# Kernel tuning notes

Measured on AMD Instinct MI355X. Metric: run time of the kernel, lower is better.

The kernel has to match this reference:

```python
import jax, jax.numpy as jnp
import numpy as np
import math

B, S, D, H, F = 2, 2048, 1024, 16, 4096
HD = D // H
EPS = 1e-5

def _alibi_slopes(n_heads):
    # n_heads is a power of 2 here (16): m_i = start * start**i, start = 2^(-2^(-(log2(n)-3)))
    start = 2.0 ** (-(2.0 ** (-(math.log2(n_heads) - 3))))
    return np.array([start * (start ** i) for i in range(n_heads)], dtype=np.float32)

SLOPES = jnp.asarray(_alibi_slopes(H))  # (H,)


def setup_inputs() -> dict:
    key = jax.random.key(0)
    ks = jax.random.split(key, 8)
    s = 0.02
    return {
        "x":  jax.random.normal(ks[0], (B, S, D), jnp.float32),
        "Wq": jax.random.normal(ks[1], (D, D), jnp.float32) * s,
        "Wk": jax.random.normal(ks[2], (D, D), jnp.float32) * s,
        "Wv": jax.random.normal(ks[3], (D, D), jnp.float32) * s,
        "Wo": jax.random.normal(ks[4], (D, D), jnp.float32) * s,
        "bo": jnp.zeros((D,), jnp.float32),
        "W1": jax.random.normal(ks[5], (F, D), jnp.float32) * s,
        "b1": jnp.zeros((F,), jnp.float32),
        "W2": jax.random.normal(ks[6], (D, F), jnp.float32) * s,
        "b2": jnp.zeros((D,), jnp.float32),
        "g1": jnp.ones((D,), jnp.float32),
        "be1": jnp.zeros((D,), jnp.float32),
        "g2": jnp.ones((D,), jnp.float32),
        "be2": jnp.zeros((D,), jnp.float32),
    }


def _layernorm(h, g, b):
    mu = jnp.mean(h, axis=-1, keepdims=True)
    var = jnp.mean((h - mu) ** 2, axis=-1, keepdims=True)
    return (h - mu) * jax.lax.rsqrt(var + EPS) * g + b


def reference(x, Wq, Wk, Wv, Wo, bo, W1, b1, W2, b2, g1, be1, g2, be2):
    # --- pre-norm ALiBi attention ---
    h = _layernorm(x, g1, be1)
    q = (h @ Wq.T).reshape(B, S, H, HD).transpose(0, 2, 1, 3)  # (B,H,S,HD)
    k = (h @ Wk.T).reshape(B, S, H, HD).transpose(0, 2, 1, 3)
    v = (h @ Wv.T).reshape(B, S, H, HD).transpose(0, 2, 1, 3)
    scores = jnp.einsum("bhqd,bhkd->bhqk", q, k) / math.sqrt(HD)
    pos = jnp.arange(S)
    dist = (pos[None, :] - pos[:, None]).astype(jnp.float32)      # (S,S): j - i
    bias = SLOPES[:, None, None] * dist[None, :, :]               # (H,S,S)
    attn = jax.nn.softmax(scores + bias[None], axis=-1)
    ao = jnp.einsum("bhqk,bhkd->bhqd", attn, v)
    ao = ao.transpose(0, 2, 1, 3).reshape(B, S, D) @ Wo.T + bo
    x = x + ao
    # --- pre-norm FFN ---
    h2 = _layernorm(x, g2, be2)
    ff = jax.nn.relu(h2 @ W1.T + b1) @ W2.T + b2
    return x + ff
```

## Files before the change

### kernel.cpp

```cpp
#include <hip/hip_runtime.h>
#include <hip/hip_bf16.h>
#include <stdint.h>

typedef unsigned short u16;
typedef __attribute__((ext_vector_type(8))) short short8;
typedef __attribute__((ext_vector_type(4))) float f32x4;

#define S_LEN 2048
#define D_DIM 1024
#define NHEAD 16
#define HDIM 64
#define NROWS 4096

__device__ __forceinline__ u16 f2bf(float f) {
  union { float f; uint32_t u; } c; c.f = f;
  uint32_t r = (c.u + 0x7fffu + ((c.u >> 16) & 1u)) >> 16;
  return (u16)r;
}

__device__ __forceinline__ uint32_t pack_bf2(float a, float b) {
  __hip_bfloat162 h = __float22bfloat162_rn(float2{a, b});
  union { __hip_bfloat162 h; uint32_t u; } c; c.h = h;
  return c.u;
}

__device__ __forceinline__ void gload_lds16(const void* g, void* l) {
  typedef const __attribute__((address_space(1))) unsigned int gq_t;
  typedef __attribute__((address_space(3))) unsigned int lq_t;
  __builtin_amdgcn_global_load_lds((gq_t*)(uintptr_t)g,
                                   (lq_t*)(uint32_t)(uintptr_t)l, 16, 0, 0);
}

__global__ __launch_bounds__(256) void cast_all(const float* __restrict__ Wq,
                                                const float* __restrict__ Wk,
                                                const float* __restrict__ Wv,
                                                const float* __restrict__ Wo,
                                                const float* __restrict__ W1,
                                                const float* __restrict__ W2,
                                                u16* __restrict__ wqkv,
                                                u16* __restrict__ wo,
                                                u16* __restrict__ w1,
                                                u16* __restrict__ w2) {
  int i = blockIdx.x * 256 + threadIdx.x;
  const float* src;
  u16* dst;
  int rel;
  if (i < 786432) {
    int ws = i / 262144;
    rel = i - ws * 262144;
    src = (ws == 0) ? Wq : ((ws == 1) ? Wk : Wv);
    dst = wqkv + (size_t)ws * 1048576;
  } else if (i < 1048576) {
    rel = i - 786432; src = Wo; dst = wo;
  } else if (i < 2097152) {
    rel = i - 1048576; src = W1; dst = w1;
  } else {
    rel = i - 2097152; src = W2; dst = w2;
  }
  float4 v = ((const float4*)src)[rel];
  ((ushort4*)dst)[rel] = make_ushort4(f2bf(v.x), f2bf(v.y), f2bf(v.z), f2bf(v.w));
}

__global__ __launch_bounds__(256) void ln_kernel(const float* __restrict__ x,
                                                 const float* __restrict__ g,
                                                 const float* __restrict__ be,
                                                 u16* __restrict__ out) {
  int row = blockIdx.x;
  int tid = threadIdx.x;
  const float4 v = ((const float4*)(x + (size_t)row * D_DIM))[tid];
  float s = v.x + v.y + v.z + v.w;
  float s2 = v.x * v.x + v.y * v.y + v.z * v.z + v.w * v.w;
#pragma unroll
  for (int off = 1; off < 64; off <<= 1) {
    s += __shfl_xor(s, off);
    s2 += __shfl_xor(s2, off);
  }
  __shared__ float ss[4], ss2[4];
  if ((tid & 63) == 0) { ss[tid >> 6] = s; ss2[tid >> 6] = s2; }
  __syncthreads();
  s = ss[0] + ss[1] + ss[2] + ss[3];
  s2 = ss2[0] + ss2[1] + ss2[2] + ss2[3];
  float mu = s * (1.0f / D_DIM);
  float var = s2 * (1.0f / D_DIM) - mu * mu;
  float rs = rsqrtf(var + 1e-5f);
  float4 gv = ((const float4*)g)[tid];
  float4 bv = ((const float4*)be)[tid];
  ushort4 o = make_ushort4(f2bf((v.x - mu) * rs * gv.x + bv.x),
                           f2bf((v.y - mu) * rs * gv.y + bv.y),
                           f2bf((v.z - mu) * rs * gv.z + bv.z),
                           f2bf((v.w - mu) * rs * gv.w + bv.w));
  ((ushort4*)(out + (size_t)row * D_DIM))[tid] = o;
}

template <int EPI>
__global__ __launch_bounds__(512, 2) void gemm_bt2(const u16* __restrict__ A,
                                                   const u16* __restrict__ Bw,
                                                   void* __restrict__ Cout,
                                                   const float* __restrict__ bias,
                                                   int M, int N, int K) {
  __shared__ u16 lsA[2][256 * 32];
  __shared__ u16 lsB[2][256 * 32];
  const int tid = threadIdx.x;
  const int wid = tid >> 6, lane = tid & 63;
  const int l4 = lane & 15, lh = lane >> 4;
  const int wr = wid >> 2, wc = wid & 3;
  const int nbn = N >> 8;
  const int nwg = (M >> 8) * nbn;
  const int t0 = (blockIdx.x & 7) * (nwg >> 3) + (blockIdx.x >> 3);
  const int bm = t0 / nbn, bn = t0 % nbn;

  f32x4 acc[8][4];
#pragma unroll
  for (int i = 0; i < 8; ++i)
#pragma unroll
    for (int j = 0; j < 4; ++j) acc[i][j] = (f32x4){0.f, 0.f, 0.f, 0.f};

  const int srow = lane >> 2;
  const int sblk = (lane & 3) ^ ((lane >> 3) & 3);
  const u16* Abase = A + ((size_t)bm * 256 + wid * 32 + srow) * K + sblk * 8;
  const u16* Bbase = Bw + ((size_t)bn * 256 + wid * 32 + srow) * K + sblk * 8;
  const size_t r16 = (size_t)16 * K;
#define STAGE(BUF, KT)                                              \
  {                                                                 \
    int ko = (KT) * 32;                                             \
    gload_lds16(Abase + ko, (char*)lsA[BUF] + wid * 2048);          \
    gload_lds16(Abase + r16 + ko, (char*)lsA[BUF] + wid * 2048 + 1024); \
    gload_lds16(Bbase + ko, (char*)lsB[BUF] + wid * 2048);          \
    gload_lds16(Bbase + r16 + ko, (char*)lsB[BUF] + wid * 2048 + 1024); \
  }

  const int swz = (lh ^ ((l4 >> 1) & 3)) << 4;
  int aoff[8], boff[4];
#pragma unroll
  for (int m = 0; m < 8; ++m) aoff[m] = (wr * 128 + m * 16 + l4) * 64 + swz;
#pragma unroll
  for (int n = 0; n < 4; ++n) boff[n] = (wc * 64 + n * 16 + l4) * 64 + swz;

  STAGE(0, 0);
  __syncthreads();
  int cur = 0;
  const int NT = K >> 5;

  for (int t = 0; t < NT; ++t) {
    if (t + 1 < NT) STAGE(cur ^ 1, t + 1);
    const char* La = (const char*)lsA[cur];
    const char* Lb = (const char*)lsB[cur];
    short8 aF[4], bF[4], aG[4];
#pragma unroll
    for (int m = 0; m < 4; ++m) aF[m] = *(const short8*)(La + aoff[m]);
#pragma unroll
    for (int n = 0; n < 4; ++n) bF[n] = *(const short8*)(Lb + boff[n]);
    __builtin_amdgcn_s_setprio(1);
#pragma unroll
    for (int m = 0; m < 4; ++m)
#pragma unroll
      for (int n = 0; n < 4; ++n)
        acc[m][n] = __builtin_amdgcn_mfma_f32_16x16x32_bf16(aF[m], bF[n], acc[m][n], 0, 0, 0);
    __builtin_amdgcn_s_setprio(0);
#pragma unroll
    for (int m = 0; m < 4; ++m) aG[m] = *(const short8*)(La + aoff[m + 4]);
    __builtin_amdgcn_s_setprio(1);
#pragma unroll
    for (int m = 0; m < 4; ++m)
#pragma unroll
      for (int n = 0; n < 4; ++n)
        acc[m + 4][n] = __builtin_amdgcn_mfma_f32_16x16x32_bf16(aG[m], bF[n], acc[m + 4][n], 0, 0, 0);
    __builtin_amdgcn_s_setprio(0);
    if (t + 1 < NT) __syncthreads();
    cur ^= 1;
  }

  const int row0 = bm * 256 + wr * 128 + lh * 4;
  const int col0 = bn * 256 + wc * 64 + l4;
#pragma unroll
  for (int m = 0; m < 8; ++m) {
#pragma unroll
    for (int n = 0; n < 4; ++n) {
      int col = col0 + n * 16;
#pragma unroll
      for (int r = 0; r < 4; ++r) {
        size_t idx = (size_t)(row0 + m * 16 + r) * N + col;
        float v = acc[m][n][r];
        if (EPI == 0) {
          ((u16*)Cout)[idx] = f2bf(v);
        } else {
          v += bias[col];
          ((u16*)Cout)[idx] = f2bf(v > 0.f ? v : 0.f);
        }
      }
    }
  }
#undef STAGE
}

template <int EPI>
__global__ __launch_bounds__(256) void gemm_bt(const u16* __restrict__ A,
                                               const u16* __restrict__ Bw,
                                               void* __restrict__ Cout,
                                               const float* __restrict__ bias,
                                               const float* __restrict__ resid,
                                               int M, int N, int K, int ksl) {
  __shared__ u16 lsA[128 * 64];
  __shared__ u16 lsB[128 * 64];
  const int tid = threadIdx.x;
  const int wid = tid >> 6, lane = tid & 63;
  const int l4 = lane & 15, lh = lane >> 4;
  const int nbn = N >> 7;
  const int nwgs = (M >> 7) * nbn;
  const int slice = blockIdx.x / nwgs;
  const int id0 = blockIdx.x % nwgs;
  const int t = (id0 & 7) * (nwgs >> 3) + (id0 >> 3);
  const int bm = t / nbn, bn = t % nbn;
  const int wr = wid >> 1, wc = wid & 1;
  const int Ks = K / ksl;

  f32x4 acc[4][4];
#pragma unroll
  for (int i = 0; i < 4; ++i)
#pragma unroll
    for (int j = 0; j < 4; ++j) acc[i][j] = (f32x4){0.f, 0.f, 0.f, 0.f};

  const u16* Ab = A + (size_t)bm * 128 * K + (size_t)slice * Ks;
  const u16* Bb = Bw + (size_t)bn * 128 * K + (size_t)slice * Ks;
  const int srow = (lane >> 3);
  const int scol = (lane & 7) * 8;

  for (int k0 = 0; k0 < Ks; k0 += 64) {
#pragma unroll
    for (int c = 0; c < 4; ++c) {
      int ch = wid * 4 + c;
      int row = ch * 8 + srow;
      gload_lds16(Ab + (size_t)row * K + k0 + scol, &lsA[ch * 512]);
      gload_lds16(Bb + (size_t)row * K + k0 + scol, &lsB[ch * 512]);
    }
    __syncthreads();
#pragma unroll
    for (int ks = 0; ks < 2; ++ks) {
      short8 af[4], bf[4];
#pragma unroll
      for (int i = 0; i < 4; ++i) {
        af[i] = *(const short8*)&lsA[(wr * 64 + i * 16 + l4) * 64 + ks * 32 + lh * 8];
        bf[i] = *(const short8*)&lsB[(wc * 64 + i * 16 + l4) * 64 + ks * 32 + lh * 8];
      }
#pragma unroll
      for (int i = 0; i < 4; ++i)
#pragma unroll
        for (int j = 0; j < 4; ++j)
          acc[i][j] = __builtin_amdgcn_mfma_f32_16x16x32_bf16(af[i], bf[j], acc[i][j], 0, 0, 0);
    }
    __syncthreads();
  }

  const int row0 = bm * 128 + wr * 64;
  const int col0 = bn * 128 + wc * 64;
  float* Cp = (float*)Cout + (size_t)slice * M * N;
#pragma unroll
  for (int i = 0; i < 4; ++i) {
#pragma unroll
    for (int j = 0; j < 4; ++j) {
      int col = col0 + j * 16 + l4;
#pragma unroll
      for (int r = 0; r < 4; ++r) {
        int row = row0 + i * 16 + lh * 4 + r;
        size_t idx = (size_t)row * N + col;
        float v = acc[i][j][r];
        if (EPI == 1) {
          ((float*)Cout)[idx] = v + bias[col] + resid[idx];
        } else {
          Cp[idx] = v;
        }
      }
    }
  }
}

__global__ __launch_bounds__(256) void reduce2_kernel(const float* __restrict__ p0,
                                                      const float* __restrict__ p1,
                                                      const float* __restrict__ resid,
                                                      const float* __restrict__ bias,
                                                      float* __restrict__ out) {
  for (int i = blockIdx.x * 256 + threadIdx.x; i < (NROWS * D_DIM) / 4;
       i += gridDim.x * 256) {
    float4 a = ((const float4*)p0)[i];
    float4 b = ((const float4*)p1)[i];
    float4 r = ((const float4*)resid)[i];
    float4 bb = ((const float4*)bias)[i & 255];
    float4 o;
    o.x = a.x + b.x + r.x + bb.x;
    o.y = a.y + b.y + r.y + bb.y;
    o.z = a.z + b.z + r.z + bb.z;
    o.w = a.w + b.w + r.w + bb.w;
    ((float4*)out)[i] = o;
  }
}

__global__ __launch_bounds__(256) void transpose_v(const u16* __restrict__ qkv,
                                                   u16* __restrict__ vt) {
  const int gw = blockIdx.x * 4 + (threadIdx.x >> 6);
  const int lane = threadIdx.x & 63;
  const int bh = gw >> 5;
  const int st = gw & 31;
  const int b = bh >> 4, h = bh & 15;
  const u16* src = qkv + (size_t)(b * S_LEN + st * 64) * 3072 + 2048 + h * 64 + lane;
  short8 acc8[8];
#pragma unroll
  for (int o = 0; o < 8; ++o)
#pragma unroll
    for (int i = 0; i < 8; ++i)
      acc8[o][i] = (short)src[(size_t)(o * 8 + i) * 3072];
  u16* dst = vt + ((size_t)bh * 64 + lane) * S_LEN + st * 64;
#pragma unroll
  for (int o = 0; o < 8; ++o) *(short8*)(dst + o * 8) = acc8[o];
}

__global__ __launch_bounds__(256, 4) void attn_kernel(const u16* __restrict__ qkv,
                                                      const u16* __restrict__ vt,
                                                      u16* __restrict__ ao,
                                                      float* __restrict__ pO,
                                                      float* __restrict__ pML) {
  const int id = blockIdx.x;
  const int sub = id & 63;
  const int ugrp = id >> 6;
  int h, j;
  if (ugrp < 15) { h = 15 - ugrp / 3; j = ugrp % 3; }
  else if (ugrp < 19) { h = 10 - ((ugrp - 15) >> 1); j = (ugrp - 15) & 1; }
  else { h = 27 - ugrp; j = 0; }
  const int b = sub >> 5, qt = sub & 31;
  const int bh = b * 16 + h;
  const int tid = threadIdx.x;
  const int wid = tid >> 6, lane = tid & 63;
  const int l4 = lane & 15, lh = lane >> 4;

  __shared__ u16 Kt[2][64 * 64];
  __shared__ u16 Vt[2][64 * 64];
  __shared__ u16 Pt[4][16 * 64];

  const size_t RS = 3 * D_DIM;
  const u16* base = qkv + (size_t)b * S_LEN * RS + h * HDIM;
  const u16* kbase = base + D_DIM;
  const u16* vtb = vt + (size_t)bh * HDIM * S_LEN;
  char* PtW = (char*)Pt[wid];

  short8 qf[2];
  {
    const u16* qp = base + (size_t)(qt * 64 + wid * 16 + l4) * RS + lh * 8;
    qf[0] = *(const short8*)qp;
    qf[1] = *(const short8*)(qp + 32);
  }

  int koff[4][2];
#pragma unroll
  for (int nb = 0; nb < 4; ++nb)
#pragma unroll
    for (int ks = 0; ks < 2; ++ks) {
      int row = nb * 16 + l4;
      koff[nb][ks] = row * 128 + (((ks * 32 + lh * 8) * 2) ^ ((row & 7) << 4));
    }
  int poff[2];
#pragma unroll
  for (int ks = 0; ks < 2; ++ks)
    poff[ks] = l4 * 128 + (((ks * 64 + lh * 16)) ^ ((l4 & 7) << 4));
  int pwoff[4];
#pragma unroll
  for (int nb = 0; nb < 4; ++nb)
    pwoff[nb] = l4 * 128 + (((lh * 8 + nb * 32)) ^ ((l4 & 7) << 4));

  const float slope2 = exp2f(-0.5f * (float)(h + 1)) * 1.44269504088896f;
  const float scale2 = 0.125f * 1.44269504088896f;
  const int ibase = lh * 4 - (qt * 64 + wid * 16 + l4);
  float bc[4][4];
#pragma unroll
  for (int nb = 0; nb < 4; ++nb)
#pragma unroll
    for (int r = 0; r < 4; ++r)
      bc[nb][r] = slope2 * (float)(ibase + 16 * nb + r);

  int nt = (int)ceilf(40.0f / (64.0f * slope2)) + 1;
  if (nt > 32) nt = 32;
  const int nsp = (nt + 11) / 12;
  const int ktmin = 32 - nt;
  const int hi = 31 - j * 12;
  int lo = hi - 11;
  if (lo < ktmin) lo = ktmin;

  float m = -1e30f;
  f32x4 lacc = (f32x4){0.f, 0.f, 0.f, 0.f};
  f32x4 accO[4];
#pragma unroll
  for (int nd = 0; nd < 4; ++nd) accO[nd] = (f32x4){0.f, 0.f, 0.f, 0.f};
  const short8 vones = {(short)0x3F80, (short)0x3F80, (short)0x3F80, (short)0x3F80,
                        (short)0x3F80, (short)0x3F80, (short)0x3F80, (short)0x3F80};

  const int srow = tid >> 3;
  const int sc8 = (tid & 7) * 8;
  const int swo = srow * 128 + ((sc8 * 2) ^ ((srow & 7) << 4));
  short8 kreg[2], vreg[2];
#define STAGE_LOAD(KT)                                                              \
  {                                                                                 \
    kreg[0] = *(const short8*)(kbase + (size_t)((KT)*64 + srow) * RS + sc8);        \
    kreg[1] = *(const short8*)(kbase + (size_t)((KT)*64 + srow + 32) * RS + sc8);   \
    vreg[0] = *(const short8*)(vtb + (size_t)srow * S_LEN + (KT)*64 + sc8);         \
    vreg[1] = *(const short8*)(vtb + (size_t)(srow + 32) * S_LEN + (KT)*64 + sc8);  \
  }
#define STAGE_WRITE(B)                                   \
  {                                                      \
    *(short8*)((char*)Kt[B] + swo) = kreg[0];            \
    *(short8*)((char*)Kt[B] + swo + 4096) = kreg[1];     \
    *(short8*)((char*)Vt[B] + swo) = vreg[0];            \
    *(short8*)((char*)Vt[B] + swo + 4096) = vreg[1];     \
  }

  STAGE_LOAD(hi);
  STAGE_WRITE(0);
  __syncthreads();
  int cur = 0;
  float ktoff = slope2 * 64.0f * (float)hi;
  const float dko = slope2 * 64.0f;

  for (int kt = hi; kt >= lo; --kt) {
    if (kt > lo) STAGE_LOAD(kt - 1);
    const char* Kc = (const char*)Kt[cur];
    const char* Vc = (const char*)Vt[cur];

    f32x4 sacc[4];
#pragma unroll
    for (int nb = 0; nb < 4; ++nb) sacc[nb] = (f32x4){0.f, 0.f, 0.f, 0.f};
    __builtin_amdgcn_s_setprio(1);
#pragma unroll
    for (int ks = 0; ks < 2; ++ks)
#pragma unroll
      for (int nb = 0; nb < 4; ++nb) {
        short8 kf = *(const short8*)(Kc + koff[nb][ks]);
        sacc[nb] = __builtin_amdgcn_mfma_f32_16x16x32_bf16(kf, qf[ks], sacc[nb], 0, 0, 0);
      }
    __builtin_amdgcn_s_setprio(0);

    float p[4][4];
#pragma unroll
    for (int nb = 0; nb < 4; ++nb)
#pragma unroll
      for (int r = 0; r < 4; ++r)
        p[nb][r] = fmaf(sacc[nb][r], scale2, bc[nb][r]);

    float mx0 = fmaxf(fmaxf(p[0][0], p[0][1]), fmaxf(p[0][2], p[0][3]));
    float mx1 = fmaxf(fmaxf(p[1][0], p[1][1]), fmaxf(p[1][2], p[1][3]));
    float mx2 = fmaxf(fmaxf(p[2][0], p[2][1]), fmaxf(p[2][2], p[2][3]));
    float mx3 = fmaxf(fmaxf(p[3][0], p[3][1]), fmaxf(p[3][2], p[3][3]));
    float tm = fmaxf(fmaxf(mx0, mx1), fmaxf(mx2, mx3));
    tm = fmaxf(tm, __shfl_xor(tm, 16));
    tm = fmaxf(tm, __shfl_xor(tm, 32));

    float mm = m - ktoff;
    if (__any(tm > mm)) {
      float mn = fmaxf(mm, tm);
      float corr = exp2f(mm - mn);
      m = mn + ktoff;
      mm = mn;
      float cb[4];
#pragma unroll
      for (int r = 0; r < 4; ++r)
        cb[r] = __shfl(corr, (lane & 48) | (lh * 4 + r));
#pragma unroll
      for (int nd = 0; nd < 4; ++nd)
#pragma unroll
        for (int r = 0; r < 4; ++r) accO[nd][r] *= cb[r];
#pragma unroll
      for (int r = 0; r < 4; ++r) lacc[r] *= cb[r];
    }

#pragma unroll
    for (int nb = 0; nb < 4; ++nb)
#pragma unroll
      for (int r = 0; r < 4; ++r) p[nb][r] = exp2f(p[nb][r] - mm);

#pragma unroll
    for (int nb = 0; nb < 4; ++nb) {
      uint32_t w0 = pack_bf2(p[nb][0], p[nb][1]);
      uint32_t w1 = pack_bf2(p[nb][2], p[nb][3]);
      *(uint2*)(PtW + pwoff[nb]) = make_uint2(w0, w1);
    }
    asm volatile("s_waitcnt lgkmcnt(0)" ::: "memory");

    __builtin_amdgcn_s_setprio(1);
#pragma unroll
    for (int ks = 0; ks < 2; ++ks) {
      short8 pf = *(const short8*)(PtW + poff[ks]);
      lacc = __builtin_amdgcn_mfma_f32_16x16x32_bf16(pf, vones, lacc, 0, 0, 0);
#pragma unroll
      for (int nd = 0; nd < 4; ++nd) {
        short8 vf = *(const short8*)(Vc + koff[nd][ks]);
        accO[nd] = __builtin_amdgcn_mfma_f32_16x16x32_bf16(pf, vf, accO[nd], 0, 0, 0);
      }
    }
    __builtin_amdgcn_s_setprio(0);

    if (kt > lo) STAGE_WRITE(cur ^ 1);
    __syncthreads();
    cur ^= 1;
    ktoff -= dko;
  }

  if (nsp == 1) {
    float ib[4];
#pragma unroll
    for (int r = 0; r < 4; ++r) ib[r] = 1.0f / lacc[r];
    u16* aop = ao + ((size_t)(b * S_LEN + qt * 64 + wid * 16 + lh * 4)) * D_DIM + h * HDIM;
#pragma unroll
    for (int nd = 0; nd < 4; ++nd)
#pragma unroll
      for (int r = 0; r < 4; ++r)
        aop[(size_t)r * D_DIM + nd * 16 + l4] = f2bf(accO[nd][r] * ib[r]);
  } else {
    const int sbase = (h <= 10) ? (h - 9) * 2 : 4 + (h - 11) * 3;
    const int pidx = sub * 19 + sbase + j;
    float* Op = pO + (size_t)pidx * 4096;
#pragma unroll
    for (int nd = 0; nd < 4; ++nd)
#pragma unroll
      for (int r = 0; r < 4; ++r)
        Op[(wid * 16 + lh * 4 + r) * 64 + nd * 16 + l4] = accO[nd][r];
    float mq[4];
#pragma unroll
    for (int r = 0; r < 4; ++r)
      mq[r] = __shfl(m, (lane & 48) | (lh * 4 + r));
    if (l4 == 0) {
      float* mlp = pML + (size_t)pidx * 128 + (wid * 16 + lh * 4) * 2;
#pragma unroll
      for (int r = 0; r < 4; ++r) {
        mlp[r * 2] = mq[r];
        mlp[r * 2 + 1] = lacc[r];
      }
    }
  }
#undef STAGE_LOAD
#undef STAGE_WRITE
}

__global__ __launch_bounds__(256) void attn_combine(const float* __restrict__ pO,
                                                    const float* __restrict__ pML,
                                                    u16* __restrict__ ao) {
  const int g = blockIdx.x;
  const int sub = g & 63;
  const int h = 9 + (g >> 6);
  const int b = sub >> 5, qt = sub & 31;
  const int nsp = (h <= 10) ? 2 : 3;
  const int sbase = (h <= 10) ? (h - 9) * 2 : 4 + (h - 11) * 3;
  const int pidx0 = sub * 19 + sbase;
  const int tid = threadIdx.x;
  const int row = tid >> 2;
  const int d0 = (tid & 3) * 16;

  float mj[3], lj[3];
#pragma unroll
  for (int k = 0; k < 3; ++k) { mj[k] = -1e30f; lj[k] = 0.f; }
  for (int k = 0; k < nsp; ++k) {
    mj[k] = pML[(size_t)(pidx0 + k) * 128 + row * 2];
    lj[k] = pML[(size_t)(pidx0 + k) * 128 + row * 2 + 1];
  }
  float ms = fmaxf(mj[0], fmaxf(mj[1], mj[2]));
  float w[3];
  float lsum = 0.f;
#pragma unroll
  for (int k = 0; k < 3; ++k) {
    w[k] = exp2f(mj[k] - ms);
    lsum += w[k] * lj[k];
  }
  float inv = 1.0f / lsum;

  u16* aop = ao + ((size_t)(b * S_LEN + qt * 64 + row)) * D_DIM + h * HDIM + d0;
#pragma unroll
  for (int c = 0; c < 4; ++c) {
    float4 o = {0.f, 0.f, 0.f, 0.f};
    for (int k = 0; k < nsp; ++k) {
      const float4 v = *(const float4*)(pO + (size_t)(pidx0 + k) * 4096 + row * 64 + d0 + c * 4);
      o.x += w[k] * v.x; o.y += w[k] * v.y; o.z += w[k] * v.z; o.w += w[k] * v.w;
    }
    ushort4 u4 = make_ushort4(f2bf(o.x * inv), f2bf(o.y * inv), f2bf(o.z * inv), f2bf(o.w * inv));
    *(ushort4*)(aop + c * 4) = u4;
  }
}

extern "C" void kernel_launch(void* const* d_in, const int* in_sizes, int n_in,
                              void* d_out, int out_size, void* d_ws, size_t ws_size,
                              hipStream_t stream) {
  const float* x   = (const float*)d_in[0];
  const float* Wq  = (const float*)d_in[1];
  const float* Wk  = (const float*)d_in[2];
  const float* Wv  = (const float*)d_in[3];
  const float* Wo  = (const float*)d_in[4];
  const float* bo  = (const float*)d_in[5];
  const float* W1  = (const float*)d_in[6];
  const float* b1  = (const float*)d_in[7];
  const float* W2  = (const float*)d_in[8];
  const float* b2  = (const float*)d_in[9];
  const float* g1  = (const float*)d_in[10];
  const float* be1 = (const float*)d_in[11];
  const float* g2  = (const float*)d_in[12];
  const float* be2 = (const float*)d_in[13];

  char* p = (char*)d_ws;
  u16* wqkv = (u16*)p; p += (size_t)3072 * 1024 * 2;
  u16* wo   = (u16*)p; p += (size_t)1024 * 1024 * 2;
  u16* w1   = (u16*)p; p += (size_t)4096 * 1024 * 2;
  u16* w2   = (u16*)p; p += (size_t)4096 * 1024 * 2;
  u16* hb   = (u16*)p; p += (size_t)4096 * 1024 * 2;
  u16* qkvb = (u16*)p; p += (size_t)4096 * 3072 * 2;
  u16* aob  = (u16*)p; p += (size_t)4096 * 1024 * 2;
  float* x1 = (float*)p; p += (size_t)4096 * 1024 * 4;
  u16* h2b  = (u16*)p; p += (size_t)4096 * 1024 * 2;
  u16* ff1  = (u16*)p; p += (size_t)4096 * 4096 * 2;
  u16* vt   = ff1;
  float* pO = (float*)(ff1 + (size_t)4 * 1024 * 1024);
  float* pML = pO + (size_t)1216 * 4096;
  float* pk = (float*)hb;

  cast_all<<<12288, 256, 0, stream>>>(Wq, Wk, Wv, Wo, W1, W2, wqkv, wo, w1, w2);

  ln_kernel<<<4096, 256, 0, stream>>>(x, g1, be1, hb);
  gemm_bt2<0><<<16 * 12, 512, 0, stream>>>(hb, wqkv, qkvb, nullptr, 4096, 3072, 1024);
  transpose_v<<<256, 256, 0, stream>>>(qkvb, vt);
  attn_kernel<<<1792, 256, 0, stream>>>(qkvb, vt, aob, pO, pML);
  attn_combine<<<448, 256, 0, stream>>>(pO, pML, aob);
  gemm_bt<1><<<32 * 8, 256, 0, stream>>>(aob, wo, x1, bo, x, 4096, 1024, 1024, 1);
  ln_kernel<<<4096, 256, 0, stream>>>(x1, g2, be2, h2b);
  gemm_bt2<2><<<16 * 16, 512, 0, stream>>>(h2b, w1, ff1, b1, 4096, 4096, 1024);
  gemm_bt<3><<<2 * 32 * 8, 256, 0, stream>>>(ff1, w2, pk, nullptr, nullptr, 4096, 1024, 4096, 2);
  reduce2_kernel<<<2048, 256, 0, stream>>>(pk, pk + (size_t)4096 * 1024, x1, b2, (float*)d_out);
}
```

Baseline: 236.3 us.

## Add 256x128-tile 512-thread double-buffered GEMM for FFN down-projection

Introduces a new GEMM kernel with 256x128 output tiles, 8 waves, K-step 32 and a double-buffered LDS pipeline using direct global-to-LDS loads. It replaces the 128x128 kernel for the W2 split-K GEMM. The larger M tile raises reuse of the B operand and halves the workgroup count. The cost is more registers per thread and fewer workgroups (256) to spread across CUs.

New measurement: 234.7 us. No clear change (-0.7%).

```diff
diff --git a/kernel.cpp b/kernel.cpp
--- a/kernel.cpp
+++ b/kernel.cpp
@@ -194,6 +194,101 @@
 }
 
 template <int EPI>
+__global__ __launch_bounds__(512, 2) void gemm_bt3(const u16* __restrict__ A,
+                                                   const u16* __restrict__ Bw,
+                                                   void* __restrict__ Cout,
+                                                   const float* __restrict__ bias,
+                                                   const float* __restrict__ resid,
+                                                   int M, int N, int K, int ksl) {
+  __shared__ u16 lsA[2][256 * 32];
+  __shared__ u16 lsB[2][128 * 32];
+  const int tid = threadIdx.x;
+  const int wid = tid >> 6, lane = tid & 63;
+  const int l4 = lane & 15, lh = lane >> 4;
+  const int wr = wid >> 1, wc = wid & 1;
+  const int nbn = N >> 7;
+  const int nwgs = (M >> 8) * nbn;
+  const int slice = blockIdx.x / nwgs;
+  const int id0 = blockIdx.x % nwgs;
+  const int t0 = (id0 & 7) * (nwgs >> 3) + (id0 >> 3);
+  const int bm = t0 / nbn, bn = t0 % nbn;
+  const int Ks = K / ksl;
+
+  f32x4 acc[4][4];
+#pragma unroll
+  for (int i = 0; i < 4; ++i)
+#pragma unroll
+    for (int j = 0; j < 4; ++j) acc[i][j] = (f32x4){0.f, 0.f, 0.f, 0.f};
+
+  const int srow = lane >> 2;
+  const int sblk = (lane & 3) ^ ((lane >> 3) & 3);
+  const u16* Abase = A + ((size_t)bm * 256 + wid * 16 + srow) * K + (size_t)slice * Ks + sblk * 8;
+  const u16* Bbase = Bw + ((size_t)bn * 128 + wid * 16 + srow) * K + (size_t)slice * Ks + sblk * 8;
+  const size_t r128 = (size_t)128 * K;
+#define STAGE(BUF, KT)                                               \
+  {                                                                  \
+    int ko = (KT) * 32;                                              \
+    gload_lds16(Abase + ko, (char*)lsA[BUF] + wid * 1024);           \
+    gload_lds16(Abase + r128 + ko, (char*)lsA[BUF] + 8192 + wid * 1024); \
+    gload_lds16(Bbase + ko, (char*)lsB[BUF] + wid * 1024);           \
+  }
+
+  const int swz = (lh ^ ((l4 >> 1) & 3)) << 4;
+  int aoff[4], boff[4];
+#pragma unroll
+  for (int m = 0; m < 4; ++m) aoff[m] = (wr * 64 + m * 16 + l4) * 64 + swz;
+#pragma unroll
+  for (int n = 0; n < 4; ++n) boff[n] = (wc * 64 + n * 16 + l4) * 64 + swz;
+
+  STAGE(0, 0);
+  __syncthreads();
+  int cur = 0;
+  const int NT = Ks >> 5;
+
+  for (int t = 0; t < NT; ++t) {
+    if (t + 1 < NT) STAGE(cur ^ 1, t + 1);
+    const char* La = (const char*)lsA[cur];
+    const char* Lb = (const char*)lsB[cur];
+    short8 aF[4], bF[4];
+#pragma unroll
+    for (int m = 0; m < 4; ++m) aF[m] = *(const short8*)(La + aoff[m]);
+#pragma unroll
+    for (int n = 0; n < 4; ++n) bF[n] = *(const short8*)(Lb + boff[n]);
+    __builtin_amdgcn_s_setprio(1);
+#pragma unroll
+    for (int m = 0; m < 4; ++m)
+#pragma unroll
+      for (int n = 0; n < 4; ++n)
+        acc[m][n] = __builtin_amdgcn_mfma_f32_16x16x32_bf16(aF[m], bF[n], acc[m][n], 0, 0, 0);
+    __builtin_amdgcn_s_setprio(0);
+    if (t + 1 < NT) __syncthreads();
+    cur ^= 1;
+  }
+
+  const int row0 = bm * 256 + wr * 64 + lh * 4;
+  const int col0 = bn * 128 + wc * 64 + l4;
+  float* Cp = (float*)Cout + (size_t)slice * M * N;
+#pragma unroll
+  for (int m = 0; m < 4; ++m) {
+#pragma unroll
+    for (int n = 0; n < 4; ++n) {
+      int col = col0 + n * 16;
+#pragma unroll
+      for (int r = 0; r < 4; ++r) {
+        size_t idx = (size_t)(row0 + m * 16 + r) * N + col;
+        float v = acc[m][n][r];
+        if (EPI == 1) {
+          ((float*)Cout)[idx] = v + bias[col] + resid[idx];
+        } else {
+          Cp[idx] = v;
+        }
+      }
+    }
+  }
+#undef STAGE
+}
+
+template <int EPI>
 __global__ __launch_bounds__(256) void gemm_bt(const u16* __restrict__ A,
                                                const u16* __restrict__ Bw,
                                                void* __restrict__ Cout,
@@ -624,6 +719,6 @@
   gemm_bt<1><<<32 * 8, 256, 0, stream>>>(aob, wo, x1, bo, x, 4096, 1024, 1024, 1);
   ln_kernel<<<4096, 256, 0, stream>>>(x1, g2, be2, h2b);
   gemm_bt2<2><<<16 * 16, 512, 0, stream>>>(h2b, w1, ff1, b1, 4096, 4096, 1024);
-  gemm_bt<3><<<2 * 32 * 8, 256, 0, stream>>>(ff1, w2, pk, nullptr, nullptr, 4096, 1024, 4096, 2);
+  gemm_bt3<3><<<2 * 16 * 8, 512, 0, stream>>>(ff1, w2, pk, nullptr, nullptr, 4096, 1024, 4096, 2);
   reduce2_kernel<<<2048, 256, 0, stream>>>(pk, pk + (size_t)4096 * 1024, x1, b2, (float*)d_out);
 }
```

## Run FFN down-projection on 256x256 GEMM with split-K 4 and bf16 partials

Applied to the files above, without the earlier changes.

The second FFN GEMM (K=4096) moves from the 128x128 split-K-2 kernel with fp32 partials to the larger 256x256 double-buffered kernel. That kernel gains a split-K parameter, and this call uses 4 slices. Partial sums are now stored in bf16, and a new vectorized reduce kernel adds the 4 slices plus bias and residual. The aim is better MFMA data reuse and full-GPU occupancy on the long-K GEMM without more partial-sum traffic. The cost is reduced accuracy from rounding each partial to bf16, plus one workgroup per CU.

Measured after the change: 227.5 us. -3.7%, faster.

```diff
diff --git a/kernel.cpp b/kernel.cpp
--- a/kernel.cpp
+++ b/kernel.cpp
@@ -16,6 +16,11 @@
   union { float f; uint32_t u; } c; c.f = f;
   uint32_t r = (c.u + 0x7fffu + ((c.u >> 16) & 1u)) >> 16;
   return (u16)r;
+}
+
+__device__ __forceinline__ float bf2f(u16 v) {
+  union { uint32_t u; float f; } c; c.u = ((uint32_t)v) << 16;
+  return c.f;
 }
 
 __device__ __forceinline__ uint32_t pack_bf2(float a, float b) {
@@ -97,7 +102,7 @@
                                                    const u16* __restrict__ Bw,
                                                    void* __restrict__ Cout,
                                                    const float* __restrict__ bias,
-                                                   int M, int N, int K) {
+                                                   int M, int N, int K, int ksl) {
   __shared__ u16 lsA[2][256 * 32];
   __shared__ u16 lsB[2][256 * 32];
   const int tid = threadIdx.x;
@@ -106,8 +111,11 @@
   const int wr = wid >> 2, wc = wid & 3;
   const int nbn = N >> 8;
   const int nwg = (M >> 8) * nbn;
-  const int t0 = (blockIdx.x & 7) * (nwg >> 3) + (blockIdx.x >> 3);
+  const int slice = blockIdx.x / nwg;
+  const int id0 = blockIdx.x % nwg;
+  const int t0 = (id0 & 7) * (nwg >> 3) + (id0 >> 3);
   const int bm = t0 / nbn, bn = t0 % nbn;
+  const int Ks = K / ksl;
 
   f32x4 acc[8][4];
 #pragma unroll
@@ -117,8 +125,8 @@
 
   const int srow = lane >> 2;
   const int sblk = (lane & 3) ^ ((lane >> 3) & 3);
-  const u16* Abase = A + ((size_t)bm * 256 + wid * 32 + srow) * K + sblk * 8;
-  const u16* Bbase = Bw + ((size_t)bn * 256 + wid * 32 + srow) * K + sblk * 8;
+  const u16* Abase = A + ((size_t)bm * 256 + wid * 32 + srow) * K + (size_t)slice * Ks + sblk * 8;
+  const u16* Bbase = Bw + ((size_t)bn * 256 + wid * 32 + srow) * K + (size_t)slice * Ks + sblk * 8;
   const size_t r16 = (size_t)16 * K;
 #define STAGE(BUF, KT)                                              \
   {                                                                 \
@@ -139,7 +147,7 @@
   STAGE(0, 0);
   __syncthreads();
   int cur = 0;
-  const int NT = K >> 5;
+  const int NT = Ks >> 5;
 
   for (int t = 0; t < NT; ++t) {
     if (t + 1 < NT) STAGE(cur ^ 1, t + 1);
@@ -172,6 +180,7 @@
 
   const int row0 = bm * 256 + wr * 128 + lh * 4;
   const int col0 = bn * 256 + wc * 64 + l4;
+  u16* Cp = (u16*)Cout + (size_t)slice * M * N;
 #pragma unroll
   for (int m = 0; m < 8; ++m) {
 #pragma unroll
@@ -183,9 +192,11 @@
         float v = acc[m][n][r];
         if (EPI == 0) {
           ((u16*)Cout)[idx] = f2bf(v);
-        } else {
+        } else if (EPI == 2) {
           v += bias[col];
           ((u16*)Cout)[idx] = f2bf(v > 0.f ? v : 0.f);
+        } else {
+          Cp[idx] = f2bf(v);
         }
       }
     }
@@ -274,24 +285,29 @@
   }
 }
 
-__global__ __launch_bounds__(256) void reduce2_kernel(const float* __restrict__ p0,
-                                                      const float* __restrict__ p1,
+__global__ __launch_bounds__(256) void reduce4_kernel(const u16* __restrict__ pk,
                                                       const float* __restrict__ resid,
                                                       const float* __restrict__ bias,
                                                       float* __restrict__ out) {
-  for (int i = blockIdx.x * 256 + threadIdx.x; i < (NROWS * D_DIM) / 4;
-       i += gridDim.x * 256) {
-    float4 a = ((const float4*)p0)[i];
-    float4 b = ((const float4*)p1)[i];
-    float4 r = ((const float4*)resid)[i];
-    float4 bb = ((const float4*)bias)[i & 255];
-    float4 o;
-    o.x = a.x + b.x + r.x + bb.x;
-    o.y = a.y + b.y + r.y + bb.y;
-    o.z = a.z + b.z + r.z + bb.z;
-    o.w = a.w + b.w + r.w + bb.w;
-    ((float4*)out)[i] = o;
-  }
+  const size_t SL = (size_t)NROWS * D_DIM;
+  int i = blockIdx.x * 256 + threadIdx.x;
+  short8 p0 = *(const short8*)(pk + (size_t)i * 8);
+  short8 p1 = *(const short8*)(pk + SL + (size_t)i * 8);
+  short8 p2 = *(const short8*)(pk + 2 * SL + (size_t)i * 8);
+  short8 p3 = *(const short8*)(pk + 3 * SL + (size_t)i * 8);
+  int col = (i * 8) & (D_DIM - 1);
+  float4 b0 = *(const float4*)(bias + col);
+  float4 b1 = *(const float4*)(bias + col + 4);
+  float4 r0 = ((const float4*)resid)[i * 2];
+  float4 r1 = ((const float4*)resid)[i * 2 + 1];
+  float o[8];
+#pragma unroll
+  for (int j = 0; j < 8; ++j)
+    o[j] = bf2f((u16)p0[j]) + bf2f((u16)p1[j]) + bf2f((u16)p2[j]) + bf2f((u16)p3[j]);
+  float4 w0 = {o[0] + b0.x + r0.x, o[1] + b0.y + r0.y, o[2] + b0.z + r0.z, o[3] + b0.w + r0.w};
+  float4 w1 = {o[4] + b1.x + r1.x, o[5] + b1.y + r1.y, o[6] + b1.z + r1.z, o[7] + b1.w + r1.w};
+  ((float4*)out)[i * 2] = w0;
+  ((float4*)out)[i * 2 + 1] = w1;
 }
 
 __global__ __launch_bounds__(256) void transpose_v(const u16* __restrict__ qkv,
@@ -612,18 +628,18 @@
   u16* vt   = ff1;
   float* pO = (float*)(ff1 + (size_t)4 * 1024 * 1024);
   float* pML = pO + (size_t)1216 * 4096;
-  float* pk = (float*)hb;
+  u16* pk = hb;
 
   cast_all<<<12288, 256, 0, stream>>>(Wq, Wk, Wv, Wo, W1, W2, wqkv, wo, w1, w2);
 
   ln_kernel<<<4096, 256, 0, stream>>>(x, g1, be1, hb);
-  gemm_bt2<0><<<16 * 12, 512, 0, stream>>>(hb, wqkv, qkvb, nullptr, 4096, 3072, 1024);
+  gemm_bt2<0><<<16 * 12, 512, 0, stream>>>(hb, wqkv, qkvb, nullptr, 4096, 3072, 1024, 1);
   transpose_v<<<256, 256, 0, stream>>>(qkvb, vt);
   attn_kernel<<<1792, 256, 0, stream>>>(qkvb, vt, aob, pO, pML);
   attn_combine<<<448, 256, 0, stream>>>(pO, pML, aob);
   gemm_bt<1><<<32 * 8, 256, 0, stream>>>(aob, wo, x1, bo, x, 4096, 1024, 1024, 1);
   ln_kernel<<<4096, 256, 0, stream>>>(x1, g2, be2, h2b);
-  gemm_bt2<2><<<16 * 16, 512, 0, stream>>>(h2b, w1, ff1, b1, 4096, 4096, 1024);
-  gemm_bt<3><<<2 * 32 * 8, 256, 0, stream>>>(ff1, w2, pk, nullptr, nullptr, 4096, 1024, 4096, 2);
-  reduce2_kernel<<<2048, 256, 0, stream>>>(pk, pk + (size_t)4096 * 1024, x1, b2, (float*)d_out);
-}
+  gemm_bt2<2><<<16 * 16, 512, 0, stream>>>(h2b, w1, ff1, b1, 4096, 4096, 1024, 1);
+  gemm_bt2<3><<<4 * 64, 512, 0, stream>>>(ff1, w2, pk, nullptr, 4096, 1024, 4096, 4);
+  reduce4_kernel<<<2048, 256, 0, stream>>>(pk, x1, b2, (float*)d_out);
+}
```
